# Optimization experiments

Measured on AMD Instinct MI355X. Metric: run time of the kernel, lower is better.

The kernel has to match this reference:

```python
import jax, jax.numpy as jnp
import numpy as np

# Dimensions: S tokens, H hidden, fused QKV out = DQ + 2*DKV (MHA: DQ == DKV),
# N adapters, LoRA rank R (A buffer holds 3*R: rank-chunks for q, k, v).
S, H, R, N = 4096, 4096, 16, 8
DQ, DKV = 4096, 4096


def setup_inputs() -> dict:
    key = jax.random.key(0)
    ks = jax.random.split(key, 6)
    x = jax.random.normal(ks[0], (S, H), dtype=jnp.float32)
    W_base = jax.random.normal(ks[1], (H, DQ + 2 * DKV), dtype=jnp.float32) * 0.02
    A_qkv = jax.random.normal(ks[2], (N, H, 3 * R), dtype=jnp.float32) * 0.02
    B_q = jax.random.normal(ks[3], (N, R, DQ), dtype=jnp.float32) * 0.02
    B_kv = jax.random.normal(ks[4], (N, R, 2 * DKV), dtype=jnp.float32) * 0.02
    weight_indices = jax.random.randint(ks[5], (S,), 0, N, dtype=jnp.int32)
    return {"x": x, "weight_indices": weight_indices, "W_base": W_base,
            "A_qkv": A_qkv, "B_q": B_q, "B_kv": B_kv}


def reference(x, weight_indices, W_base, A_qkv, B_q, B_kv):
    # Base fused QKV projection: [S, DQ + 2*DKV]
    base = x @ W_base
    rank = A_qkv.shape[2] // 3
    b_dim_q = B_q.shape[2]
    b_dim_kv = B_kv.shape[2] // 2
    n_adapters = A_qkv.shape[0]

    # Per-token indexed LoRA (ldmm): for token t with adapter a = indices[t],
    #   delta[t] = (x[t] @ A[a, :, chunk]) @ B[a].
    # Delta-weight (quantized) buffers are empty (set_topping_info with None),
    # so ldmm reduces to the LoRA term. We loop over the small fixed set of
    # adapters, masking tokens, instead of gathering [S,H,3R] per-token weights.
    delta = jnp.zeros_like(base)
    for a in range(n_adapters):
        m = (weight_indices == a).astype(x.dtype)[:, None]  # [S,1]
        xa = (m * x) @ A_qkv[a]                              # [S, 3R]
        oq = xa[:, 0:rank] @ B_q[a]                          # [S, DQ]
        ok = xa[:, rank:2 * rank] @ B_kv[a][:, :b_dim_kv]    # [S, DKV]
        ov = xa[:, 2 * rank:3 * rank] @ B_kv[a][:, b_dim_kv:]
        delta = delta.at[:, 0:b_dim_q].add(oq)
        delta = delta.at[:, b_dim_kv:2 * b_dim_kv].add(ok)
        delta = delta.at[:, 2 * b_dim_kv:3 * b_dim_kv].add(ov)
    return base + delta
```

## Files before the change

kernel.cpp:

```cpp
#include <hip/hip_runtime.h>

#define S_TOK 4096
#define H_DIM 4096
#define NOUT  12288
#define KBIG  4480
#define NADP  8
#define RANK  16
#define NT    (KBIG / 64)

typedef __bf16 bf16x8 __attribute__((ext_vector_type(8)));
typedef float  f32x4  __attribute__((ext_vector_type(4)));

__device__ __forceinline__ unsigned short f2bf(float f) {
  union { float f; unsigned int u; } v; v.f = f;
  unsigned int u = v.u;
  unsigned int r = (u + 0x7FFFu + ((u >> 16) & 1u)) >> 16;
  return (unsigned short)r;
}

__device__ __forceinline__ void gload_lds16(const void* g, void* l) {
  __builtin_amdgcn_global_load_lds(
      (const __attribute__((address_space(1))) void*)g,
      (__attribute__((address_space(3))) void*)l,
      16, 0, 0);
}

#define WT_BLOCKS 12288
#define CX_BLOCKS 4096
#define TA_BLOCKS 256
#define BF_BLOCKS 1536
__global__ __launch_bounds__(256) void prep_fused(
    const float* __restrict__ W, const float* __restrict__ x,
    const float* __restrict__ A, const float* __restrict__ Bq,
    const float* __restrict__ Bkv, unsigned short* __restrict__ WbigT,
    unsigned short* __restrict__ xbig, unsigned short* __restrict__ AT) {
  __shared__ float smem[128 * 49];
  const int b = blockIdx.x;
  const int tid = threadIdx.x;

  if (b < WT_BLOCKS) {
    float (*tile)[65] = (float(*)[65])smem;
    const int n0 = (b % 192) * 64;
    const int k0 = (b / 192) * 64;
    const int c = tid & 63;
    const int rb = tid >> 6;
#pragma unroll
    for (int p = 0; p < 16; ++p) {
      int r = p * 4 + rb;
      tile[r][c] = W[(size_t)(k0 + r) * NOUT + n0 + c];
    }
    __syncthreads();
#pragma unroll
    for (int p = 0; p < 16; ++p) {
      int nr = p * 4 + rb;
      WbigT[(size_t)(n0 + nr) * KBIG + k0 + c] = f2bf(tile[c][nr]);
    }
  } else if (b < WT_BLOCKS + CX_BLOCKS) {
    const int t = b - WT_BLOCKS;
    const float4* xr = (const float4*)(x + (size_t)t * H_DIM);
    ushort4* o = (ushort4*)(xbig + (size_t)t * KBIG);
#pragma unroll
    for (int p = 0; p < 4; ++p) {
      float4 v = xr[p * 256 + tid];
      ushort4 u;
      u.x = f2bf(v.x); u.y = f2bf(v.y); u.z = f2bf(v.z); u.w = f2bf(v.w);
      o[p * 256 + tid] = u;
    }
  } else if (b < WT_BLOCKS + CX_BLOCKS + TA_BLOCKS) {
    const int bb = b - (WT_BLOCKS + CX_BLOCKS);
    const int a = bb >> 5;
    const int h0 = (bb & 31) * 128;
    float (*t)[49] = (float(*)[49])smem;
    const float* src = A + ((size_t)a * H_DIM + h0) * 48;
#pragma unroll
    for (int e = 0; e < 24; ++e) {
      int idx = e * 256 + tid;
      t[idx / 48][idx % 48] = src[idx];
    }
    __syncthreads();
#pragma unroll
    for (int e = 0; e < 24; ++e) {
      int idx = e * 256 + tid;
      int j = idx >> 7;
      int c = idx & 127;
      AT[(size_t)(a * 48 + j) * H_DIM + h0 + c] = f2bf(t[c][j]);
    }
  } else {
    const int bb = b - (WT_BLOCKS + CX_BLOCKS + TA_BLOCKS);
#pragma unroll
    for (int e = 0; e < 12; ++e) {
      int idx = e * 256 + tid;
      int n = bb * 8 + (idx / 384);
      int c = idx % 384;
      int a = c / 48, j = c % 48;
      float v = 0.0f;
      if (j < 16) {
        if (n < 4096) v = Bq[(size_t)(a * RANK + j) * 4096 + n];
      } else if (j < 32) {
        if (n >= 4096 && n < 8192) v = Bkv[(size_t)(a * RANK + (j - 16)) * 8192 + (n - 4096)];
      } else {
        if (n >= 8192) v = Bkv[(size_t)(a * RANK + (j - 32)) * 8192 + (n - 4096)];
      }
      WbigT[(size_t)n * KBIG + H_DIM + c] = f2bf(v);
    }
  }
}

__global__ __launch_bounds__(256) void xa_gemm_scatter(
    const unsigned short* __restrict__ Xb, const unsigned short* __restrict__ AT,
    const int* __restrict__ widx, unsigned short* __restrict__ xbig) {
  __shared__ __align__(16) unsigned char lds[16384 + 8192];
  const int tid = threadIdx.x;
  const int w = tid >> 6, l = tid & 63;
  const int wm = w >> 1, wn = w & 1;
  const int lr = l & 15, hi = l >> 4;
  const int innsw = (lr & 7) << 4;
  const int m0 = blockIdx.y * 128;
  const int n0 = blockIdx.x * 64;

  f32x4 acc[4][2];
  const f32x4 fzero = {0.f, 0.f, 0.f, 0.f};
#pragma unroll
  for (int mf = 0; mf < 4; ++mf)
#pragma unroll
    for (int nf = 0; nf < 2; ++nf) acc[mf][nf] = fzero;

  for (int kt = 0; kt < H_DIM / 64; ++kt) {
    __syncthreads();
    const int kb = kt * 64;
#pragma unroll
    for (int ld = 0; ld < 4; ++ld) {
      int d = (ld * 256 + tid) * 16;
      int row = d >> 7;
      int colb = (d & 127) ^ ((row & 7) << 4);
      gload_lds16((const char*)Xb + (size_t)(m0 + row) * (KBIG * 2) + kb * 2 + colb,
                  &lds[d]);
    }
#pragma unroll
    for (int ld = 0; ld < 2; ++ld) {
      int d = (ld * 256 + tid) * 16;
      int row = d >> 7;
      int colb = (d & 127) ^ ((row & 7) << 4);
      gload_lds16((const char*)AT + (size_t)(n0 + row) * (H_DIM * 2) + kb * 2 + colb,
                  &lds[16384 + d]);
    }
    __syncthreads();
#pragma unroll
    for (int kk = 0; kk < 2; ++kk) {
      bf16x8 af[4], bfr[2];
#pragma unroll
      for (int mf = 0; mf < 4; ++mf)
        af[mf] = *(const bf16x8*)(lds + (wm * 64 + mf * 16 + lr) * 128 +
                                  ((kk * 64 + hi * 16) ^ innsw));
#pragma unroll
      for (int nf = 0; nf < 2; ++nf)
        bfr[nf] = *(const bf16x8*)(lds + 16384 + (wn * 32 + nf * 16 + lr) * 128 +
                                   ((kk * 64 + hi * 16) ^ innsw));
#pragma unroll
      for (int mf = 0; mf < 4; ++mf)
#pragma unroll
        for (int nf = 0; nf < 2; ++nf)
          acc[mf][nf] = __builtin_amdgcn_mfma_f32_16x16x32_bf16(
              af[mf], bfr[nf], acc[mf][nf], 0, 0, 0);
    }
  }
  const int r4 = hi * 4;
#pragma unroll
  for (int mf = 0; mf < 4; ++mf)
#pragma unroll
    for (int r = 0; r < 4; ++r) {
      const int t = m0 + wm * 64 + mf * 16 + r4 + r;
      const int a = widx[t];
#pragma unroll
      for (int nf = 0; nf < 2; ++nf) {
        const int col = n0 + wn * 32 + nf * 16 + lr;
        float v = (col / 48 == a) ? acc[mf][nf][r] : 0.0f;
        xbig[(size_t)t * KBIG + H_DIM + col] = f2bf(v);
      }
    }
}

__global__ __launch_bounds__(512, 2) void gemm_bf16_8ph(
    const unsigned short* __restrict__ Xb, const unsigned short* __restrict__ Wt,
    float* __restrict__ out) {
  __shared__ __align__(16) unsigned char lds[2 * 2 * 2 * 16384];

  const int tid = threadIdx.x;
  const int w   = tid >> 6;
  const int l   = tid & 63;
  const int wm  = w >> 2;
  const int wn  = w & 3;
  const int lr  = l & 15;
  const int hi  = l >> 4;
  const int innsw = (lr & 7) << 4;

  const int id  = blockIdx.x;
  const int swz = (id & 7) * 96 + (id >> 3);
  const int bm = swz / 48, bn = swz % 48;
  const int m0 = bm * 256, n0 = bn * 256;

  auto stage = [&](int buf, int ab, int half, const unsigned short* G,
                   int row0, int kb) {
    unsigned char* lb = &lds[((((buf << 1) | ab) << 1) | half) * 16384];
    const char* gb = (const char*)G;
#pragma unroll
    for (int ld = 0; ld < 2; ++ld) {
      int d = (ld * 512 + tid) * 16;
      int row = d >> 7;
      int colb = (d & 127) ^ ((row & 7) << 4);
      gload_lds16(gb + (size_t)(row0 + row) * (KBIG * 2) + kb * 2 + colb,
                  lb + d);
    }
  };
  auto readA = [&](int buf, int mq, int mf, int kk) -> bf16x8 {
    const unsigned char* lb = &lds[((((buf << 1) | 0) << 1) | mq) * 16384];
    int ph = (wm * 64 + mf * 16 + lr) * 128 + ((kk * 64 + hi * 16) ^ innsw);
    return *(const bf16x8*)(lb + ph);
  };
  auto readB = [&](int buf, int nq, int nf, int kk) -> bf16x8 {
    const unsigned char* lb = &lds[((((buf << 1) | 1) << 1) | nq) * 16384];
    int ph = (wn * 32 + nf * 16 + lr) * 128 + ((kk * 64 + hi * 16) ^ innsw);
    return *(const bf16x8*)(lb + ph);
  };

  f32x4 acc[4][4][2];
  const f32x4 fzero = {0.f, 0.f, 0.f, 0.f};
#pragma unroll
  for (int q = 0; q < 4; ++q)
#pragma unroll
    for (int mf = 0; mf < 4; ++mf)
#pragma unroll
      for (int nf = 0; nf < 2; ++nf) acc[q][mf][nf] = fzero;

  bf16x8 a_[4][2];
  bf16x8 b0_[2][2];
  bf16x8 b1_[2][2];

#define MFMA_QUAD(Q, BSRC)                                                   \
    _Pragma("unroll") for (int kk = 0; kk < 2; ++kk)                         \
      _Pragma("unroll") for (int mf = 0; mf < 4; ++mf)                       \
        _Pragma("unroll") for (int nf = 0; nf < 2; ++nf)                     \
          acc[Q][mf][nf] = __builtin_amdgcn_mfma_f32_16x16x32_bf16(          \
              a_[mf][kk], BSRC[nf][kk], acc[Q][mf][nf], 0, 0, 0)

  stage(0, 0, 0, Xb, m0,       0);
  stage(0, 1, 0, Wt, n0,       0);
  stage(0, 1, 1, Wt, n0 + 128, 0);
  stage(0, 0, 1, Xb, m0 + 128, 0);

  for (int t = 0; t < NT; ++t) {
    const int cur = t & 1, nxt = cur ^ 1;
    const int tn = (t + 1 < NT) ? (t + 1) : t;
    const int kb_next = tn * 64;

    asm volatile("s_waitcnt vmcnt(2)" ::: "memory");
    __builtin_amdgcn_s_barrier();

#pragma unroll
    for (int mf = 0; mf < 4; ++mf)
#pragma unroll
      for (int kk = 0; kk < 2; ++kk) a_[mf][kk] = readA(cur, 0, mf, kk);
#pragma unroll
    for (int nf = 0; nf < 2; ++nf)
#pragma unroll
      for (int kk = 0; kk < 2; ++kk) b0_[nf][kk] = readB(cur, 0, nf, kk);
#pragma unroll
    for (int nf = 0; nf < 2; ++nf)
#pragma unroll
      for (int kk = 0; kk < 2; ++kk) b1_[nf][kk] = readB(cur, 1, nf, kk);
    stage(nxt, 0, 0, Xb, m0, kb_next);
    stage(nxt, 1, 0, Wt, n0, kb_next);
    __builtin_amdgcn_s_setprio(1);
    MFMA_QUAD(0, b0_);
    MFMA_QUAD(1, b1_);
    __builtin_amdgcn_s_setprio(0);

    asm volatile("s_waitcnt vmcnt(4)" ::: "memory");
    __builtin_amdgcn_s_barrier();

#pragma unroll
    for (int mf = 0; mf < 4; ++mf)
#pragma unroll
      for (int kk = 0; kk < 2; ++kk) a_[mf][kk] = readA(cur, 1, mf, kk);
    stage(nxt, 1, 1, Wt, n0 + 128, kb_next);
    stage(nxt, 0, 1, Xb, m0 + 128, kb_next);
    __builtin_amdgcn_s_setprio(1);
    MFMA_QUAD(2, b1_);
    MFMA_QUAD(3, b0_);
    __builtin_amdgcn_s_setprio(0);
  }
#undef MFMA_QUAD

  const int r4 = hi * 4;
  constexpr int QM[4] = {0, 0, 1, 1};
  constexpr int QN[4] = {0, 1, 1, 0};
#pragma unroll
  for (int q = 0; q < 4; ++q)
#pragma unroll
    for (int mf = 0; mf < 4; ++mf)
#pragma unroll
      for (int nf = 0; nf < 2; ++nf) {
        const int row = m0 + QM[q] * 128 + wm * 64 + mf * 16 + r4;
        const int col = n0 + QN[q] * 128 + wn * 32 + nf * 16 + lr;
#pragma unroll
        for (int r = 0; r < 4; ++r)
          out[(size_t)(row + r) * NOUT + col] = acc[q][mf][nf][r];
      }
}

extern "C" void kernel_launch(void* const* d_in, const int* in_sizes, int n_in,
                              void* d_out, int out_size, void* d_ws, size_t ws_size,
                              hipStream_t stream) {
  const float* x    = (const float*)d_in[0];
  const int*   widx = (const int*)d_in[1];
  const float* W    = (const float*)d_in[2];
  const float* Aq   = (const float*)d_in[3];
  const float* Bq   = (const float*)d_in[4];
  const float* Bkv  = (const float*)d_in[5];
  float* out = (float*)d_out;

  unsigned short* xbig  = (unsigned short*)d_ws;
  unsigned short* WbigT = (unsigned short*)((char*)d_ws + (size_t)S_TOK * KBIG * 2);
  unsigned short* AT    = (unsigned short*)((char*)d_ws + (size_t)S_TOK * KBIG * 2
                                            + (size_t)NOUT * KBIG * 2);

  hipLaunchKernelGGL(prep_fused, dim3(WT_BLOCKS + CX_BLOCKS + TA_BLOCKS + BF_BLOCKS),
                     dim3(256), 0, stream, W, x, Aq, Bq, Bkv, WbigT, xbig, AT);
  hipLaunchKernelGGL(xa_gemm_scatter, dim3(6, S_TOK / 128), dim3(256), 0, stream,
                     xbig, AT, widx, xbig);
  hipLaunchKernelGGL(gemm_bf16_8ph, dim3(768), dim3(512), 0, stream, xbig, WbigT, out);
}
```

Baseline: 480.9 us.

## Fuse LoRA xA GEMM into prep kernel, reading fp32 x and A directly

The separate A-transpose pass and the xa_gemm_scatter kernel are folded into the prep kernel as 192 leading blocks. These blocks load fp32 x and A from global memory, convert to bf16 in registers, and write the results into swizzled LDS. This removes one kernel launch, the AT workspace and the dependency on the bf16 x copy. The xA blocks now use plain per-thread loads, and for A these are strided scalar reads, instead of async global_load_lds. They run 64 k-iterations each and may become a long tail inside the prep kernel.

```diff
diff --git a/kernel.cpp b/kernel.cpp
--- a/kernel.cpp
+++ b/kernel.cpp
@@ -25,23 +25,101 @@
       16, 0, 0);
 }
 
+#define XA_BLOCKS 192
 #define WT_BLOCKS 12288
 #define CX_BLOCKS 4096
-#define TA_BLOCKS 256
 #define BF_BLOCKS 1536
-__global__ __launch_bounds__(256) void prep_fused(
+#define TOTAL_BLOCKS (XA_BLOCKS + WT_BLOCKS + CX_BLOCKS + BF_BLOCKS)
+
+__global__ __launch_bounds__(256) void prep_mega(
     const float* __restrict__ W, const float* __restrict__ x,
     const float* __restrict__ A, const float* __restrict__ Bq,
-    const float* __restrict__ Bkv, unsigned short* __restrict__ WbigT,
-    unsigned short* __restrict__ xbig, unsigned short* __restrict__ AT) {
-  __shared__ float smem[128 * 49];
+    const float* __restrict__ Bkv, const int* __restrict__ widx,
+    unsigned short* __restrict__ WbigT, unsigned short* __restrict__ xbig) {
+  __shared__ __align__(16) float smem[128 * 49];
   const int b = blockIdx.x;
   const int tid = threadIdx.x;
 
-  if (b < WT_BLOCKS) {
+  if (b < XA_BLOCKS) {
+    unsigned char* lds8 = (unsigned char*)smem;
+    const int m0 = (b / 6) * 128;
+    const int n0 = (b % 6) * 64;
+    const int w = tid >> 6, l = tid & 63;
+    const int wm = w >> 1, wn = w & 1;
+    const int lr = l & 15, hi = l >> 4;
+    const int innsw = (lr & 7) << 4;
+
+    f32x4 acc[4][2];
+    const f32x4 fzero = {0.f, 0.f, 0.f, 0.f};
+#pragma unroll
+    for (int mf = 0; mf < 4; ++mf)
+#pragma unroll
+      for (int nf = 0; nf < 2; ++nf) acc[mf][nf] = fzero;
+
+    const int xrow = tid >> 4;
+    const int xc4  = tid & 15;
+    const int arow = tid >> 6;
+    const int ah   = tid & 63;
+
+    for (int kt = 0; kt < H_DIM / 64; ++kt) {
+      const int kb = kt * 64;
+      __syncthreads();
+#pragma unroll
+      for (int p = 0; p < 8; ++p) {
+        const int row = p * 16 + xrow;
+        float4 v = *(const float4*)(x + (size_t)(m0 + row) * H_DIM + kb + xc4 * 4);
+        uint2 pk;
+        pk.x = (unsigned)f2bf(v.x) | ((unsigned)f2bf(v.y) << 16);
+        pk.y = (unsigned)f2bf(v.z) | ((unsigned)f2bf(v.w) << 16);
+        *(uint2*)(lds8 + row * 128 + ((xc4 * 8) ^ ((row & 7) << 4))) = pk;
+      }
+#pragma unroll
+      for (int p = 0; p < 16; ++p) {
+        const int row = p * 4 + arow;
+        const int jj = n0 + row;
+        const int a = jj / 48, j = jj - a * 48;
+        float v = A[((size_t)a * H_DIM + kb + ah) * 48 + j];
+        *(unsigned short*)(lds8 + 16384 + row * 128 + ((ah * 2) ^ ((row & 7) << 4))) = f2bf(v);
+      }
+      __syncthreads();
+#pragma unroll
+      for (int kk = 0; kk < 2; ++kk) {
+        bf16x8 af[4], bfr[2];
+#pragma unroll
+        for (int mf = 0; mf < 4; ++mf)
+          af[mf] = *(const bf16x8*)(lds8 + (wm * 64 + mf * 16 + lr) * 128 +
+                                    ((kk * 64 + hi * 16) ^ innsw));
+#pragma unroll
+        for (int nf = 0; nf < 2; ++nf)
+          bfr[nf] = *(const bf16x8*)(lds8 + 16384 + (wn * 32 + nf * 16 + lr) * 128 +
+                                     ((kk * 64 + hi * 16) ^ innsw));
+#pragma unroll
+        for (int mf = 0; mf < 4; ++mf)
+#pragma unroll
+          for (int nf = 0; nf < 2; ++nf)
+            acc[mf][nf] = __builtin_amdgcn_mfma_f32_16x16x32_bf16(
+                af[mf], bfr[nf], acc[mf][nf], 0, 0, 0);
+      }
+    }
+    const int r4 = hi * 4;
+#pragma unroll
+    for (int mf = 0; mf < 4; ++mf)
+#pragma unroll
+      for (int r = 0; r < 4; ++r) {
+        const int t = m0 + wm * 64 + mf * 16 + r4 + r;
+        const int a = widx[t];
+#pragma unroll
+        for (int nf = 0; nf < 2; ++nf) {
+          const int col = n0 + wn * 32 + nf * 16 + lr;
+          float v = (col / 48 == a) ? acc[mf][nf][r] : 0.0f;
+          xbig[(size_t)t * KBIG + H_DIM + col] = f2bf(v);
+        }
+      }
+  } else if (b < XA_BLOCKS + WT_BLOCKS) {
+    const int bb = b - XA_BLOCKS;
     float (*tile)[65] = (float(*)[65])smem;
-    const int n0 = (b % 192) * 64;
-    const int k0 = (b / 192) * 64;
+    const int n0 = (bb % 192) * 64;
+    const int k0 = (bb / 192) * 64;
     const int c = tid & 63;
     const int rb = tid >> 6;
 #pragma unroll
@@ -55,8 +133,8 @@
       int nr = p * 4 + rb;
       WbigT[(size_t)(n0 + nr) * KBIG + k0 + c] = f2bf(tile[c][nr]);
     }
-  } else if (b < WT_BLOCKS + CX_BLOCKS) {
-    const int t = b - WT_BLOCKS;
+  } else if (b < XA_BLOCKS + WT_BLOCKS + CX_BLOCKS) {
+    const int t = b - (XA_BLOCKS + WT_BLOCKS);
     const float4* xr = (const float4*)(x + (size_t)t * H_DIM);
     ushort4* o = (ushort4*)(xbig + (size_t)t * KBIG);
 #pragma unroll
@@ -66,27 +144,8 @@
       u.x = f2bf(v.x); u.y = f2bf(v.y); u.z = f2bf(v.z); u.w = f2bf(v.w);
       o[p * 256 + tid] = u;
     }
-  } else if (b < WT_BLOCKS + CX_BLOCKS + TA_BLOCKS) {
-    const int bb = b - (WT_BLOCKS + CX_BLOCKS);
-    const int a = bb >> 5;
-    const int h0 = (bb & 31) * 128;
-    float (*t)[49] = (float(*)[49])smem;
-    const float* src = A + ((size_t)a * H_DIM + h0) * 48;
-#pragma unroll
-    for (int e = 0; e < 24; ++e) {
-      int idx = e * 256 + tid;
-      t[idx / 48][idx % 48] = src[idx];
-    }
-    __syncthreads();
-#pragma unroll
-    for (int e = 0; e < 24; ++e) {
-      int idx = e * 256 + tid;
-      int j = idx >> 7;
-      int c = idx & 127;
-      AT[(size_t)(a * 48 + j) * H_DIM + h0 + c] = f2bf(t[c][j]);
-    }
   } else {
-    const int bb = b - (WT_BLOCKS + CX_BLOCKS + TA_BLOCKS);
+    const int bb = b - (XA_BLOCKS + WT_BLOCKS + CX_BLOCKS);
 #pragma unroll
     for (int e = 0; e < 12; ++e) {
       int idx = e * 256 + tid;
@@ -106,80 +165,6 @@
   }
 }
 
-__global__ __launch_bounds__(256) void xa_gemm_scatter(
-    const unsigned short* __restrict__ Xb, const unsigned short* __restrict__ AT,
-    const int* __restrict__ widx, unsigned short* __restrict__ xbig) {
-  __shared__ __align__(16) unsigned char lds[16384 + 8192];
-  const int tid = threadIdx.x;
-  const int w = tid >> 6, l = tid & 63;
-  const int wm = w >> 1, wn = w & 1;
-  const int lr = l & 15, hi = l >> 4;
-  const int innsw = (lr & 7) << 4;
-  const int m0 = blockIdx.y * 128;
-  const int n0 = blockIdx.x * 64;
-
-  f32x4 acc[4][2];
-  const f32x4 fzero = {0.f, 0.f, 0.f, 0.f};
-#pragma unroll
-  for (int mf = 0; mf < 4; ++mf)
-#pragma unroll
-    for (int nf = 0; nf < 2; ++nf) acc[mf][nf] = fzero;
-
-  for (int kt = 0; kt < H_DIM / 64; ++kt) {
-    __syncthreads();
-    const int kb = kt * 64;
-#pragma unroll
-    for (int ld = 0; ld < 4; ++ld) {
-      int d = (ld * 256 + tid) * 16;
-      int row = d >> 7;
-      int colb = (d & 127) ^ ((row & 7) << 4);
-      gload_lds16((const char*)Xb + (size_t)(m0 + row) * (KBIG * 2) + kb * 2 + colb,
-                  &lds[d]);
-    }
-#pragma unroll
-    for (int ld = 0; ld < 2; ++ld) {
-      int d = (ld * 256 + tid) * 16;
-      int row = d >> 7;
-      int colb = (d & 127) ^ ((row & 7) << 4);
-      gload_lds16((const char*)AT + (size_t)(n0 + row) * (H_DIM * 2) + kb * 2 + colb,
-                  &lds[16384 + d]);
-    }
-    __syncthreads();
-#pragma unroll
-    for (int kk = 0; kk < 2; ++kk) {
-      bf16x8 af[4], bfr[2];
-#pragma unroll
-      for (int mf = 0; mf < 4; ++mf)
-        af[mf] = *(const bf16x8*)(lds + (wm * 64 + mf * 16 + lr) * 128 +
-                                  ((kk * 64 + hi * 16) ^ innsw));
-#pragma unroll
-      for (int nf = 0; nf < 2; ++nf)
-        bfr[nf] = *(const bf16x8*)(lds + 16384 + (wn * 32 + nf * 16 + lr) * 128 +
-                                   ((kk * 64 + hi * 16) ^ innsw));
-#pragma unroll
-      for (int mf = 0; mf < 4; ++mf)
-#pragma unroll
-        for (int nf = 0; nf < 2; ++nf)
-          acc[mf][nf] = __builtin_amdgcn_mfma_f32_16x16x32_bf16(
-              af[mf], bfr[nf], acc[mf][nf], 0, 0, 0);
-    }
-  }
-  const int r4 = hi * 4;
-#pragma unroll
-  for (int mf = 0; mf < 4; ++mf)
-#pragma unroll
-    for (int r = 0; r < 4; ++r) {
-      const int t = m0 + wm * 64 + mf * 16 + r4 + r;
-      const int a = widx[t];
-#pragma unroll
-      for (int nf = 0; nf < 2; ++nf) {
-        const int col = n0 + wn * 32 + nf * 16 + lr;
-        float v = (col / 48 == a) ? acc[mf][nf][r] : 0.0f;
-        xbig[(size_t)t * KBIG + H_DIM + col] = f2bf(v);
-      }
-    }
-}
-
 __global__ __launch_bounds__(512, 2) void gemm_bf16_8ph(
     const unsigned short* __restrict__ Xb, const unsigned short* __restrict__ Wt,
     float* __restrict__ out) {
@@ -321,12 +306,8 @@
 
   unsigned short* xbig  = (unsigned short*)d_ws;
   unsigned short* WbigT = (unsigned short*)((char*)d_ws + (size_t)S_TOK * KBIG * 2);
-  unsigned short* AT    = (unsigned short*)((char*)d_ws + (size_t)S_TOK * KBIG * 2
-                                            + (size_t)NOUT * KBIG * 2);
-
-  hipLaunchKernelGGL(prep_fused, dim3(WT_BLOCKS + CX_BLOCKS + TA_BLOCKS + BF_BLOCKS),
-                     dim3(256), 0, stream, W, x, Aq, Bq, Bkv, WbigT, xbig, AT);
-  hipLaunchKernelGGL(xa_gemm_scatter, dim3(6, S_TOK / 128), dim3(256), 0, stream,
-                     xbig, AT, widx, xbig);
+
+  hipLaunchKernelGGL(prep_mega, dim3(TOTAL_BLOCKS), dim3(256), 0, stream,
+                     W, x, Aq, Bq, Bkv, widx, WbigT, xbig);
   hipLaunchKernelGGL(gemm_bf16_8ph, dim3(768), dim3(512), 0, stream, xbig, WbigT, out);
 }
```

Result: slower. 572.6 us (+19.1%).
